# Kernel tuning notes

Hardware: AMD Instinct MI355X
Metric: run time of the kernel (lower is better)

The kernel has to match this reference:

```python
import jax, jax.numpy as jnp
import numpy as np

N_NODES = 100000
N_HYPEREDGES = 20000
NNZ = 600000
D = 128


def setup_inputs() -> dict:
    key = jax.random.key(0)
    k = jax.random.split(key, 6)
    s = 1.0 / np.sqrt(D)
    x = jax.random.normal(k[0], (N_NODES, D), jnp.float32)
    node_idx = jax.random.randint(k[1], (NNZ,), 0, N_NODES, dtype=jnp.int64 if jax.config.jax_enable_x64 else jnp.int32)
    edge_idx = jax.random.randint(k[2], (NNZ,), 0, N_HYPEREDGES, dtype=jnp.int64 if jax.config.jax_enable_x64 else jnp.int32)
    conv_W = jax.random.uniform(k[3], (D, D), jnp.float32, -s, s)
    conv_b = jnp.zeros((D,), jnp.float32)
    res_W = jax.random.uniform(k[4], (D, D), jnp.float32, -s, s)
    res_b = jax.random.uniform(k[5], (D,), jnp.float32, -s, s)
    return {"x": x, "node_idx": node_idx, "edge_idx": edge_idx,
            "conv_W": conv_W, "conv_b": conv_b, "res_W": res_W, "res_b": res_b}


def hypergraph_conv(x, node_idx, edge_idx, W, b):
    # PyG HypergraphConv (no attention, unit hyperedge weights):
    #   out = D^{-1} H B^{-1} H^T (x W) + b
    y = x @ W                                                      # [N, D]
    ones = jnp.ones(node_idx.shape, dtype=y.dtype)
    deg_n = jax.ops.segment_sum(ones, node_idx, num_segments=N_NODES)        # node degree
    deg_e = jax.ops.segment_sum(ones, edge_idx, num_segments=N_HYPEREDGES)   # hyperedge size
    inv_n = jnp.where(deg_n > 0, 1.0 / deg_n, 0.0)
    inv_e = jnp.where(deg_e > 0, 1.0 / deg_e, 0.0)
    # node -> hyperedge aggregation, normalized by B^{-1}
    e_feat = jax.ops.segment_sum(y[node_idx], edge_idx, num_segments=N_HYPEREDGES)
    e_feat = e_feat * inv_e[:, None]                               # [E, D]
    # hyperedge -> node aggregation, normalized by D^{-1}
    out = jax.ops.segment_sum(e_feat[edge_idx], node_idx, num_segments=N_NODES)
    out = out * inv_n[:, None]                                     # [N, D]
    return out + b


def reference(x, node_idx, edge_idx, conv_W, conv_b, res_W, res_b):
    h = hypergraph_conv(x, node_idx, edge_idx, conv_W, conv_b)     # layer_num = 1
    return (x @ res_W + res_b) + h                                 # residual Linear + conv out
```

## Files before the change

kernel.cpp:

```cpp
#include <hip/hip_runtime.h>

#define N_NODES 100000
#define N_EDGES 20000
#define NNZ_C   600000
#define D 128

typedef short bf16x8 __attribute__((ext_vector_type(8)));
typedef float f32x4  __attribute__((ext_vector_type(4)));

__device__ __forceinline__ unsigned short f2bf(float f) {
    unsigned int u = __float_as_uint(f);
    u = (u + 0x7fffu + ((u >> 16) & 1u)) >> 16;
    return (unsigned short)u;
}
__device__ __forceinline__ float bf2f(unsigned short h) {
    return __uint_as_float((unsigned int)h << 16);
}
__device__ __forceinline__ unsigned int pk_trunc(float lo, float hi) {
    return __builtin_amdgcn_perm(__float_as_uint(hi), __float_as_uint(lo),
                                 0x07060302);
}

#define CH 2048
#define NCHUNK 293
#define EBW 32
#define NBE 625
#define ECAP 1280
#define NBW 128
#define NBN 782
#define NCAP 1024
#define PADI 32
#define GCUR_INTS ((NBE + NBN) * PADI)

#define GT 64
#define XPAD 136
#define NTILES ((N_NODES + GT - 1) / GT)
#define GEMM_BLKS ((NTILES + 1) / 2)

__device__ __forceinline__ void stage_tile(unsigned short* __restrict__ buf,
                                           const float* __restrict__ x,
                                           int tile, int r0, int qp) {
    int n = tile * GT + r0;
    if (n >= N_NODES) n = N_NODES - 1;
    const float* xr = x + (size_t)n * D + qp * 16;
    unsigned short* dst = buf + r0 * XPAD + qp * 16;
#pragma unroll
    for (int u = 0; u < 2; ++u) {
        const float4 a = *(const float4*)(xr + u * 8);
        const float4 c = *(const float4*)(xr + u * 8 + 4);
        uint4 v;
        v.x = pk_trunc(a.x, a.y);
        v.y = pk_trunc(a.z, a.w);
        v.z = pk_trunc(c.x, c.y);
        v.w = pk_trunc(c.z, c.w);
        *(uint4*)(dst + u * 8) = v;
    }
}

__device__ __forceinline__ void compute_tile(
    const unsigned short* __restrict__ buf, const bf16x8 (&A)[2][4],
    int tile, int mat, int fh, int quad, int l16,
    unsigned short* __restrict__ yb, unsigned short* __restrict__ resb) {
    f32x4 acc[4][2] = {};
#pragma unroll
    for (int g = 0; g < 4; ++g)
#pragma unroll
        for (int kc = 0; kc < 4; ++kc) {
            const bf16x8 B = *(const bf16x8*)(buf + (g * 16 + l16) * XPAD +
                                              kc * 32 + quad * 8);
            acc[g][0] = __builtin_amdgcn_mfma_f32_16x16x32_bf16(A[0][kc], B, acc[g][0], 0, 0, 0);
            acc[g][1] = __builtin_amdgcn_mfma_f32_16x16x32_bf16(A[1][kc], B, acc[g][1], 0, 0, 0);
        }
    const int nbase = tile * GT;
    unsigned short* dst = mat ? resb : yb;
#pragma unroll
    for (int g = 0; g < 4; ++g) {
        const int n = nbase + g * 16 + l16;
        if (n >= N_NODES) continue;
#pragma unroll
        for (int ft = 0; ft < 2; ++ft) {
            const int f0 = fh + ft * 16 + quad * 4;
            uint2 v;
            v.x = pk_trunc(acc[g][ft][0], acc[g][ft][1]);
            v.y = pk_trunc(acc[g][ft][2], acc[g][ft][3]);
            *(uint2*)(dst + (size_t)n * D + f0) = v;
        }
    }
}

__global__ __launch_bounds__(512) void fused_bin_gemm(
    const float* __restrict__ x,
    const int* __restrict__ nidx, const int* __restrict__ eidx,
    const float* __restrict__ cW, const float* __restrict__ rW,
    unsigned short* __restrict__ yb, unsigned short* __restrict__ resb,
    int* __restrict__ bucket_e, int* __restrict__ bucket_n,
    int* __restrict__ gcur_e, int* __restrict__ gcur_n) {
    __shared__ int lds[10816];
    const int bid = blockIdx.x;
    const int tid = threadIdx.x;

    if (bid < NCHUNK) {
        int* rawE  = lds;
        int* rawN  = lds + 2048;
        int* srt   = lds + 4096;
        int* red   = lds + 6144;
        int* cnt   = lds + 6656;
        int* lbase = lds + 7438;
        int* gbase = lds + 8220;
        int* cur   = lds + 9002;
        unsigned short* sbin = (unsigned short*)(lds + 9784);
        const int j0 = bid * CH;
        const int jn = (j0 + CH < NNZ_C) ? CH : NNZ_C - j0;
        for (int i = tid; i < jn; i += 512) {
            rawE[i] = eidx[j0 + i];
            rawN[i] = nidx[j0 + i];
        }
        __syncthreads();
#pragma unroll
        for (int s = 0; s < 2; ++s) {
            const int nb = s ? NBN : NBE;
            int* gc = s ? gcur_n : gcur_e;
            int* dst = s ? bucket_n : bucket_e;
            const int cap = s ? NCAP : ECAP;
            for (int i = tid; i < nb; i += 512) cnt[i] = 0;
            __syncthreads();
            for (int i = tid; i < jn; i += 512)
                atomicAdd(&cnt[s ? (rawN[i] >> 7) : (rawE[i] >> 5)], 1);
            __syncthreads();
            const int i0 = tid * 2, i1 = tid * 2 + 1;
            const int a0 = (i0 < nb) ? cnt[i0] : 0;
            const int a1 = (i1 < nb) ? cnt[i1] : 0;
            const int sum = a0 + a1;
            red[tid] = sum;
            __syncthreads();
            for (int off = 1; off < 512; off <<= 1) {
                const int t = (tid >= off) ? red[tid - off] : 0;
                __syncthreads();
                red[tid] += t;
                __syncthreads();
            }
            const int excl = red[tid] - sum;
            if (i0 < nb) {
                lbase[i0] = excl; cur[i0] = excl;
                gbase[i0] = a0 ? atomicAdd(&gc[i0 * PADI], a0) : 0;
            }
            if (i1 < nb) {
                lbase[i1] = excl + a0; cur[i1] = excl + a0;
                gbase[i1] = a1 ? atomicAdd(&gc[i1 * PADI], a1) : 0;
            }
            __syncthreads();
            for (int i = tid; i < jn; i += 512) {
                const int e = rawE[i], n = rawN[i];
                const int b = s ? (n >> 7) : (e >> 5);
                const int pk = s ? (((n & 127) << 15) | e)
                                 : (((e & 31) << 17) | n);
                const int pos = atomicAdd(&cur[b], 1);
                srt[pos] = pk;
                sbin[pos] = (unsigned short)b;
            }
            __syncthreads();
            for (int i = tid; i < jn; i += 512) {
                const int b = sbin[i];
                const int o2 = gbase[b] + (i - lbase[b]);
                if (o2 < cap) dst[b * cap + o2] = srt[i];
            }
            __syncthreads();
        }
        return;
    }

    unsigned short* xs0 = (unsigned short*)lds;
    unsigned short* xs1 = xs0 + GT * XPAD;

    const int w    = tid >> 6;
    const int lane = tid & 63;
    const int quad = lane >> 4;
    const int l16  = lane & 15;
    const int mat  = w & 1;
    const int fh   = (w >> 1) * 32;
    const int r0 = tid >> 3;
    const int qp = tid & 7;
    const int t0 = (bid - NCHUNK) * 2;

    stage_tile(xs0, x, t0, r0, qp);

    const float* wf = mat ? rW : cW;
    bf16x8 A[2][4];
#pragma unroll
    for (int ft = 0; ft < 2; ++ft) {
        const int f = fh + ft * 16 + l16;
#pragma unroll
        for (int kc = 0; kc < 4; ++kc)
#pragma unroll
            for (int u = 0; u < 8; ++u)
                A[ft][kc][u] = (short)f2bf(wf[(kc * 32 + quad * 8 + u) * D + f]);
    }
    __syncthreads();
    stage_tile(xs1, x, t0 + 1, r0, qp);
    compute_tile(xs0, A, t0, mat, fh, quad, l16, yb, resb);
    __syncthreads();
    compute_tile(xs1, A, t0 + 1, mat, fh, quad, l16, yb, resb);
}

__global__ __launch_bounds__(512) void edge_aggregate(
    const int* __restrict__ bucket_e, const int* __restrict__ gcur_e,
    const unsigned short* __restrict__ yb, unsigned short* __restrict__ efb) {
    __shared__ int raw[ECAP];
    __shared__ int srt[ECAP];
    __shared__ int cnt[EBW + 1];
    __shared__ int cur[EBW];
    const int tid = threadIdx.x;
    const int b = blockIdx.x;
    int W = gcur_e[b * PADI];
    if (W > ECAP) W = ECAP;
    if (tid <= EBW) cnt[tid] = 0;
    __syncthreads();
    const int* src = bucket_e + b * ECAP;
    for (int i = tid; i < W; i += 512) {
        const int p = src[i];
        raw[i] = p;
        atomicAdd(&cnt[p >> 17], 1);
    }
    __syncthreads();
    if (tid < EBW) {
        const int c = cnt[tid];
        int v = c;
#pragma unroll
        for (int off = 1; off < EBW; off <<= 1) {
            const int t = __shfl_up(v, off);
            if (tid >= off) v += t;
        }
        cnt[tid] = v - c;
        cur[tid] = v - c;
        if (tid == EBW - 1) cnt[EBW] = v;
    }
    __syncthreads();
    for (int i = tid; i < W; i += 512) {
        const int p = raw[i];
        const int pos = atomicAdd(&cur[p >> 17], 1);
        srt[pos] = p & 0x1FFFF;
    }
    __syncthreads();

    const int g = tid >> 4;
    const int l = tid & 15;
    const int beg = cnt[g], end = cnt[g + 1];
    float acc[8] = {};
    int j = beg;
    for (; j + 4 <= end; j += 4) {
        const int n0 = srt[j], n1 = srt[j + 1];
        const int n2 = srt[j + 2], n3 = srt[j + 3];
        const bf16x8 p0 = *(const bf16x8*)(yb + (size_t)n0 * D + l * 8);
        const bf16x8 p1 = *(const bf16x8*)(yb + (size_t)n1 * D + l * 8);
        const bf16x8 p2 = *(const bf16x8*)(yb + (size_t)n2 * D + l * 8);
        const bf16x8 p3 = *(const bf16x8*)(yb + (size_t)n3 * D + l * 8);
#pragma unroll
        for (int i = 0; i < 8; ++i)
            acc[i] += (bf2f((unsigned short)p0[i]) + bf2f((unsigned short)p1[i]))
                    + (bf2f((unsigned short)p2[i]) + bf2f((unsigned short)p3[i]));
    }
    for (; j < end; ++j) {
        const bf16x8 p = *(const bf16x8*)(yb + (size_t)srt[j] * D + l * 8);
#pragma unroll
        for (int i = 0; i < 8; ++i) acc[i] += bf2f((unsigned short)p[i]);
    }
    const int deg = end - beg;
    const float inv = deg ? 1.f / (float)deg : 0.f;
    bf16x8 o;
#pragma unroll
    for (int i = 0; i < 8; ++i) o[i] = (short)f2bf(acc[i] * inv);
    *(bf16x8*)(efb + (size_t)(b * EBW + g) * D + l * 8) = o;
}

__global__ __launch_bounds__(512) void node_aggregate(
    const int* __restrict__ bucket_n, const int* __restrict__ gcur_n,
    const unsigned short* __restrict__ efb, const unsigned short* __restrict__ resb,
    const float* __restrict__ rb, const float* __restrict__ cb,
    float* __restrict__ out) {
    __shared__ int raw[NCAP];
    __shared__ int srt[NCAP];
    __shared__ int cnt[NBW + 1];
    __shared__ int cur[NBW];
    __shared__ int red[512];
    const int tid = threadIdx.x;
    const int b = blockIdx.x;
    int W = gcur_n[b * PADI];
    if (W > NCAP) W = NCAP;
    if (tid <= NBW) cnt[tid] = 0;
    __syncthreads();
    const int* src = bucket_n + b * NCAP;
    for (int i = tid; i < W; i += 512) {
        const int p = src[i];
        raw[i] = p;
        atomicAdd(&cnt[p >> 15], 1);
    }
    __syncthreads();
    const int v = (tid < NBW) ? cnt[tid] : 0;
    red[tid] = v;
    __syncthreads();
    for (int off = 1; off < 512; off <<= 1) {
        const int t = (tid >= off) ? red[tid - off] : 0;
        __syncthreads();
        red[tid] += t;
        __syncthreads();
    }
    const int excl = red[tid] - v;
    if (tid < NBW) { cnt[tid] = excl; cur[tid] = excl; }
    if (tid == NBW - 1) cnt[NBW] = red[tid];
    __syncthreads();
    for (int i = tid; i < W; i += 512) {
        const int p = raw[i];
        const int pos = atomicAdd(&cur[p >> 15], 1);
        srt[pos] = p & 0x7FFF;
    }
    __syncthreads();

    const int g = tid >> 4;
    const int l = tid & 15;
    const float4 rb0 = *(const float4*)(rb + l * 8);
    const float4 rb1 = *(const float4*)(rb + l * 8 + 4);
    const float4 cb0 = *(const float4*)(cb + l * 8);
    const float4 cb1 = *(const float4*)(cb + l * 8 + 4);
#pragma unroll
    for (int u = 0; u < 4; ++u) {
        const int nl = g * 4 + u;
        const int n = b * NBW + nl;
        if (n >= N_NODES) continue;
        const int beg = cnt[nl], end = cnt[nl + 1];
        float acc[8] = {};
        int j = beg;
        for (; j + 2 <= end; j += 2) {
            const int e0 = srt[j], e1 = srt[j + 1];
            const bf16x8 p0 = *(const bf16x8*)(efb + (size_t)e0 * D + l * 8);
            const bf16x8 p1 = *(const bf16x8*)(efb + (size_t)e1 * D + l * 8);
#pragma unroll
            for (int i = 0; i < 8; ++i)
                acc[i] += bf2f((unsigned short)p0[i]) + bf2f((unsigned short)p1[i]);
        }
        if (j < end) {
            const bf16x8 p = *(const bf16x8*)(efb + (size_t)srt[j] * D + l * 8);
#pragma unroll
            for (int i = 0; i < 8; ++i) acc[i] += bf2f((unsigned short)p[i]);
        }
        const int deg = end - beg;
        const float inv = deg ? 1.f / (float)deg : 0.f;
        const bf16x8 r = *(const bf16x8*)(resb + (size_t)n * D + l * 8);
        float4 o0, o1;
        o0.x = bf2f((unsigned short)r[0]) + acc[0] * inv + rb0.x + cb0.x;
        o0.y = bf2f((unsigned short)r[1]) + acc[1] * inv + rb0.y + cb0.y;
        o0.z = bf2f((unsigned short)r[2]) + acc[2] * inv + rb0.z + cb0.z;
        o0.w = bf2f((unsigned short)r[3]) + acc[3] * inv + rb0.w + cb0.w;
        o1.x = bf2f((unsigned short)r[4]) + acc[4] * inv + rb1.x + cb1.x;
        o1.y = bf2f((unsigned short)r[5]) + acc[5] * inv + rb1.y + cb1.y;
        o1.z = bf2f((unsigned short)r[6]) + acc[6] * inv + rb1.z + cb1.z;
        o1.w = bf2f((unsigned short)r[7]) + acc[7] * inv + rb1.w + cb1.w;
        const size_t o = (size_t)n * D + l * 8;
        *(float4*)(out + o) = o0;
        *(float4*)(out + o + 4) = o1;
    }
}

extern "C" void kernel_launch(void* const* d_in, const int* in_sizes, int n_in,
                              void* d_out, int out_size, void* d_ws,
                              size_t ws_size, hipStream_t stream) {
    const float* x  = (const float*)d_in[0];
    const int* nidx = (const int*)d_in[1];
    const int* eidx = (const int*)d_in[2];
    const float* cW = (const float*)d_in[3];
    const float* cb = (const float*)d_in[4];
    const float* rW = (const float*)d_in[5];
    const float* rb = (const float*)d_in[6];
    float* out = (float*)d_out;

    char* ws = (char*)d_ws;
    size_t off = 0;
    auto alloc = [&](size_t bytes) {
        size_t o = off;
        off += (bytes + 255) & ~(size_t)255;
        return o;
    };
    unsigned short* yb   = (unsigned short*)(ws + alloc((size_t)N_NODES * D * 2));
    unsigned short* resb = (unsigned short*)(ws + alloc((size_t)N_NODES * D * 2));
    unsigned short* efb  = (unsigned short*)(ws + alloc((size_t)N_EDGES * D * 2));
    int* bucket_e = (int*)(ws + alloc((size_t)NBE * ECAP * 4));
    int* bucket_n = (int*)(ws + alloc((size_t)NBN * NCAP * 4));
    int* gcur     = (int*)(ws + alloc((size_t)GCUR_INTS * 4));
    int* gcur_e = gcur;
    int* gcur_n = gcur + NBE * PADI;

    hipMemsetAsync(gcur, 0, (size_t)GCUR_INTS * 4, stream);

    fused_bin_gemm<<<NCHUNK + GEMM_BLKS, 512, 0, stream>>>(
        x, nidx, eidx, cW, rW, yb, resb,
        bucket_e, bucket_n, gcur_e, gcur_n);

    edge_aggregate<<<NBE, 512, 0, stream>>>(bucket_e, gcur_e, yb, efb);
    node_aggregate<<<NBN, 512, 0, stream>>>(bucket_n, gcur_n, efb, resb,
                                            rb, cb, out);
}
```

Measured before the change: 197.9 us.

## Aggregate raw bf16 features first and apply both GEMMs in one final pass

Uses linearity to move the conv weight multiply after both mean aggregations. The first kernel now only bins indices and converts x to bf16, the two gather kernels average raw features, and a final MFMA kernel computes z·Wc + x·Wr + biases in one pass. This removes the separate yb/resb buffers and the residual re-read in the node kernel, but adds a zb write and read plus an extra launch. The binning chunk size is also doubled, and the block scans now use warp shuffles instead of LDS-based scans.

```diff
diff --git a/kernel.cpp b/kernel.cpp
--- a/kernel.cpp
+++ b/kernel.cpp
@@ -21,8 +21,9 @@
                                  0x07060302);
 }
 
-#define CH 2048
-#define NCHUNK 293
+#define CH 4096
+#define NCHUNK 147
+#define CONVB 256
 #define EBW 32
 #define NBE 625
 #define ECAP 1280
@@ -35,176 +36,103 @@
 #define GT 64
 #define XPAD 136
 #define NTILES ((N_NODES + GT - 1) / GT)
-#define GEMM_BLKS ((NTILES + 1) / 2)
-
-__device__ __forceinline__ void stage_tile(unsigned short* __restrict__ buf,
-                                           const float* __restrict__ x,
-                                           int tile, int r0, int qp) {
-    int n = tile * GT + r0;
-    if (n >= N_NODES) n = N_NODES - 1;
-    const float* xr = x + (size_t)n * D + qp * 16;
-    unsigned short* dst = buf + r0 * XPAD + qp * 16;
-#pragma unroll
-    for (int u = 0; u < 2; ++u) {
-        const float4 a = *(const float4*)(xr + u * 8);
-        const float4 c = *(const float4*)(xr + u * 8 + 4);
-        uint4 v;
-        v.x = pk_trunc(a.x, a.y);
-        v.y = pk_trunc(a.z, a.w);
-        v.z = pk_trunc(c.x, c.y);
-        v.w = pk_trunc(c.z, c.w);
-        *(uint4*)(dst + u * 8) = v;
-    }
-}
-
-__device__ __forceinline__ void compute_tile(
-    const unsigned short* __restrict__ buf, const bf16x8 (&A)[2][4],
-    int tile, int mat, int fh, int quad, int l16,
-    unsigned short* __restrict__ yb, unsigned short* __restrict__ resb) {
-    f32x4 acc[4][2] = {};
-#pragma unroll
-    for (int g = 0; g < 4; ++g)
-#pragma unroll
-        for (int kc = 0; kc < 4; ++kc) {
-            const bf16x8 B = *(const bf16x8*)(buf + (g * 16 + l16) * XPAD +
-                                              kc * 32 + quad * 8);
-            acc[g][0] = __builtin_amdgcn_mfma_f32_16x16x32_bf16(A[0][kc], B, acc[g][0], 0, 0, 0);
-            acc[g][1] = __builtin_amdgcn_mfma_f32_16x16x32_bf16(A[1][kc], B, acc[g][1], 0, 0, 0);
-        }
-    const int nbase = tile * GT;
-    unsigned short* dst = mat ? resb : yb;
-#pragma unroll
-    for (int g = 0; g < 4; ++g) {
-        const int n = nbase + g * 16 + l16;
-        if (n >= N_NODES) continue;
-#pragma unroll
-        for (int ft = 0; ft < 2; ++ft) {
-            const int f0 = fh + ft * 16 + quad * 4;
-            uint2 v;
-            v.x = pk_trunc(acc[g][ft][0], acc[g][ft][1]);
-            v.y = pk_trunc(acc[g][ft][2], acc[g][ft][3]);
-            *(uint2*)(dst + (size_t)n * D + f0) = v;
-        }
-    }
-}
-
-__global__ __launch_bounds__(512) void fused_bin_gemm(
+#define TPB 3
+#define GEMM_BLKS ((NTILES + TPB - 1) / TPB)
+
+__global__ __launch_bounds__(512) void fused_bin_conv(
     const float* __restrict__ x,
     const int* __restrict__ nidx, const int* __restrict__ eidx,
-    const float* __restrict__ cW, const float* __restrict__ rW,
-    unsigned short* __restrict__ yb, unsigned short* __restrict__ resb,
+    unsigned short* __restrict__ xb,
     int* __restrict__ bucket_e, int* __restrict__ bucket_n,
     int* __restrict__ gcur_e, int* __restrict__ gcur_n) {
-    __shared__ int lds[10816];
+    __shared__ int srt[CH];
+    __shared__ int cnt[NBN], lbase[NBN], gbase[NBN], cur[NBN];
     const int bid = blockIdx.x;
     const int tid = threadIdx.x;
 
-    if (bid < NCHUNK) {
-        int* rawE  = lds;
-        int* rawN  = lds + 2048;
-        int* srt   = lds + 4096;
-        int* red   = lds + 6144;
-        int* cnt   = lds + 6656;
-        int* lbase = lds + 7438;
-        int* gbase = lds + 8220;
-        int* cur   = lds + 9002;
-        unsigned short* sbin = (unsigned short*)(lds + 9784);
-        const int j0 = bid * CH;
-        const int jn = (j0 + CH < NNZ_C) ? CH : NNZ_C - j0;
+    if (bid >= NCHUNK) {
+        const int total8 = N_NODES * D / 8;
+        for (int g = (bid - NCHUNK) * 512 + tid; g < total8;
+             g += CONVB * 512) {
+            const float4 a = *(const float4*)(x + (size_t)g * 8);
+            const float4 c = *(const float4*)(x + (size_t)g * 8 + 4);
+            uint4 v;
+            v.x = pk_trunc(a.x, a.y);
+            v.y = pk_trunc(a.z, a.w);
+            v.z = pk_trunc(c.x, c.y);
+            v.w = pk_trunc(c.z, c.w);
+            *(uint4*)(xb + (size_t)g * 8) = v;
+        }
+        return;
+    }
+
+    const int j0 = bid * CH;
+    const int jn = (j0 + CH < NNZ_C) ? CH : NNZ_C - j0;
+#pragma unroll
+    for (int s = 0; s < 2; ++s) {
+        const int nb = s ? NBN : NBE;
+        int* gc = s ? gcur_n : gcur_e;
+        int* dst = s ? bucket_n : bucket_e;
+        const int cap = s ? NCAP : ECAP;
+        for (int i = tid; i < nb; i += 512) cnt[i] = 0;
+        __syncthreads();
         for (int i = tid; i < jn; i += 512) {
-            rawE[i] = eidx[j0 + i];
-            rawN[i] = nidx[j0 + i];
-        }
-        __syncthreads();
-#pragma unroll
-        for (int s = 0; s < 2; ++s) {
-            const int nb = s ? NBN : NBE;
-            int* gc = s ? gcur_n : gcur_e;
-            int* dst = s ? bucket_n : bucket_e;
-            const int cap = s ? NCAP : ECAP;
-            for (int i = tid; i < nb; i += 512) cnt[i] = 0;
-            __syncthreads();
-            for (int i = tid; i < jn; i += 512)
-                atomicAdd(&cnt[s ? (rawN[i] >> 7) : (rawE[i] >> 5)], 1);
-            __syncthreads();
-            const int i0 = tid * 2, i1 = tid * 2 + 1;
-            const int a0 = (i0 < nb) ? cnt[i0] : 0;
-            const int a1 = (i1 < nb) ? cnt[i1] : 0;
-            const int sum = a0 + a1;
-            red[tid] = sum;
-            __syncthreads();
-            for (int off = 1; off < 512; off <<= 1) {
-                const int t = (tid >= off) ? red[tid - off] : 0;
-                __syncthreads();
-                red[tid] += t;
-                __syncthreads();
+            const int id = s ? nidx[j0 + i] : eidx[j0 + i];
+            atomicAdd(&cnt[s ? (id >> 7) : (id >> 5)], 1);
+        }
+        __syncthreads();
+        if (tid < 64) {
+            int loc[13];
+            int ssum = 0;
+            const int k0 = tid * 13;
+#pragma unroll
+            for (int k = 0; k < 13; ++k) {
+                const int idx = k0 + k;
+                loc[k] = ssum;
+                if (idx < nb) ssum += cnt[idx];
             }
-            const int excl = red[tid] - sum;
-            if (i0 < nb) {
-                lbase[i0] = excl; cur[i0] = excl;
-                gbase[i0] = a0 ? atomicAdd(&gc[i0 * PADI], a0) : 0;
+            int v = ssum;
+#pragma unroll
+            for (int off = 1; off < 64; off <<= 1) {
+                const int t = __shfl_up(v, off);
+                if (tid >= off) v += t;
             }
-            if (i1 < nb) {
-                lbase[i1] = excl + a0; cur[i1] = excl + a0;
-                gbase[i1] = a1 ? atomicAdd(&gc[i1 * PADI], a1) : 0;
+            const int base = v - ssum;
+#pragma unroll
+            for (int k = 0; k < 13; ++k) {
+                const int idx = k0 + k;
+                if (idx < nb) {
+                    lbase[idx] = base + loc[k];
+                    cur[idx] = base + loc[k];
+                }
             }
-            __syncthreads();
-            for (int i = tid; i < jn; i += 512) {
-                const int e = rawE[i], n = rawN[i];
-                const int b = s ? (n >> 7) : (e >> 5);
-                const int pk = s ? (((n & 127) << 15) | e)
-                                 : (((e & 31) << 17) | n);
-                const int pos = atomicAdd(&cur[b], 1);
-                srt[pos] = pk;
-                sbin[pos] = (unsigned short)b;
-            }
-            __syncthreads();
-            for (int i = tid; i < jn; i += 512) {
-                const int b = sbin[i];
-                const int o2 = gbase[b] + (i - lbase[b]);
-                if (o2 < cap) dst[b * cap + o2] = srt[i];
-            }
-            __syncthreads();
-        }
-        return;
-    }
-
-    unsigned short* xs0 = (unsigned short*)lds;
-    unsigned short* xs1 = xs0 + GT * XPAD;
-
-    const int w    = tid >> 6;
-    const int lane = tid & 63;
-    const int quad = lane >> 4;
-    const int l16  = lane & 15;
-    const int mat  = w & 1;
-    const int fh   = (w >> 1) * 32;
-    const int r0 = tid >> 3;
-    const int qp = tid & 7;
-    const int t0 = (bid - NCHUNK) * 2;
-
-    stage_tile(xs0, x, t0, r0, qp);
-
-    const float* wf = mat ? rW : cW;
-    bf16x8 A[2][4];
-#pragma unroll
-    for (int ft = 0; ft < 2; ++ft) {
-        const int f = fh + ft * 16 + l16;
-#pragma unroll
-        for (int kc = 0; kc < 4; ++kc)
-#pragma unroll
-            for (int u = 0; u < 8; ++u)
-                A[ft][kc][u] = (short)f2bf(wf[(kc * 32 + quad * 8 + u) * D + f]);
-    }
-    __syncthreads();
-    stage_tile(xs1, x, t0 + 1, r0, qp);
-    compute_tile(xs0, A, t0, mat, fh, quad, l16, yb, resb);
-    __syncthreads();
-    compute_tile(xs1, A, t0 + 1, mat, fh, quad, l16, yb, resb);
-}
-
-__global__ __launch_bounds__(512) void edge_aggregate(
+        }
+        __syncthreads();
+        for (int i = tid; i < nb; i += 512)
+            gbase[i] = cnt[i] ? atomicAdd(&gc[i * PADI], cnt[i]) : 0;
+        __syncthreads();
+        for (int i = tid; i < jn; i += 512) {
+            const int e = eidx[j0 + i], n = nidx[j0 + i];
+            const int b = s ? (n >> 7) : (e >> 5);
+            const unsigned pk = s ? (unsigned)(((n & 127) << 15) | e)
+                                  : (unsigned)(((e & 31) << 17) | n);
+            const int pos = atomicAdd(&cur[b], 1);
+            srt[pos] = (int)(pk | ((unsigned)b << 22));
+        }
+        __syncthreads();
+        for (int i = tid; i < jn; i += 512) {
+            const unsigned v = (unsigned)srt[i];
+            const int b = v >> 22;
+            const int o2 = gbase[b] + (i - lbase[b]);
+            if (o2 < cap) dst[b * cap + o2] = (int)(v & 0x3FFFFFu);
+        }
+        __syncthreads();
+    }
+}
+
+__global__ __launch_bounds__(512) void edge_mean(
     const int* __restrict__ bucket_e, const int* __restrict__ gcur_e,
-    const unsigned short* __restrict__ yb, unsigned short* __restrict__ efb) {
+    const unsigned short* __restrict__ xb, unsigned short* __restrict__ sb) {
     __shared__ int raw[ECAP];
     __shared__ int srt[ECAP];
     __shared__ int cnt[EBW + 1];
@@ -250,17 +178,17 @@
     for (; j + 4 <= end; j += 4) {
         const int n0 = srt[j], n1 = srt[j + 1];
         const int n2 = srt[j + 2], n3 = srt[j + 3];
-        const bf16x8 p0 = *(const bf16x8*)(yb + (size_t)n0 * D + l * 8);
-        const bf16x8 p1 = *(const bf16x8*)(yb + (size_t)n1 * D + l * 8);
-        const bf16x8 p2 = *(const bf16x8*)(yb + (size_t)n2 * D + l * 8);
-        const bf16x8 p3 = *(const bf16x8*)(yb + (size_t)n3 * D + l * 8);
+        const bf16x8 p0 = *(const bf16x8*)(xb + (size_t)n0 * D + l * 8);
+        const bf16x8 p1 = *(const bf16x8*)(xb + (size_t)n1 * D + l * 8);
+        const bf16x8 p2 = *(const bf16x8*)(xb + (size_t)n2 * D + l * 8);
+        const bf16x8 p3 = *(const bf16x8*)(xb + (size_t)n3 * D + l * 8);
 #pragma unroll
         for (int i = 0; i < 8; ++i)
             acc[i] += (bf2f((unsigned short)p0[i]) + bf2f((unsigned short)p1[i]))
                     + (bf2f((unsigned short)p2[i]) + bf2f((unsigned short)p3[i]));
     }
     for (; j < end; ++j) {
-        const bf16x8 p = *(const bf16x8*)(yb + (size_t)srt[j] * D + l * 8);
+        const bf16x8 p = *(const bf16x8*)(xb + (size_t)srt[j] * D + l * 8);
 #pragma unroll
         for (int i = 0; i < 8; ++i) acc[i] += bf2f((unsigned short)p[i]);
     }
@@ -269,19 +197,16 @@
     bf16x8 o;
 #pragma unroll
     for (int i = 0; i < 8; ++i) o[i] = (short)f2bf(acc[i] * inv);
-    *(bf16x8*)(efb + (size_t)(b * EBW + g) * D + l * 8) = o;
-}
-
-__global__ __launch_bounds__(512) void node_aggregate(
+    *(bf16x8*)(sb + (size_t)(b * EBW + g) * D + l * 8) = o;
+}
+
+__global__ __launch_bounds__(512) void node_mean(
     const int* __restrict__ bucket_n, const int* __restrict__ gcur_n,
-    const unsigned short* __restrict__ efb, const unsigned short* __restrict__ resb,
-    const float* __restrict__ rb, const float* __restrict__ cb,
-    float* __restrict__ out) {
+    const unsigned short* __restrict__ sb, unsigned short* __restrict__ zb) {
     __shared__ int raw[NCAP];
     __shared__ int srt[NCAP];
     __shared__ int cnt[NBW + 1];
     __shared__ int cur[NBW];
-    __shared__ int red[512];
     const int tid = threadIdx.x;
     const int b = blockIdx.x;
     int W = gcur_n[b * PADI];
@@ -295,18 +220,20 @@
         atomicAdd(&cnt[p >> 15], 1);
     }
     __syncthreads();
-    const int v = (tid < NBW) ? cnt[tid] : 0;
-    red[tid] = v;
-    __syncthreads();
-    for (int off = 1; off < 512; off <<= 1) {
-        const int t = (tid >= off) ? red[tid - off] : 0;
-        __syncthreads();
-        red[tid] += t;
-        __syncthreads();
-    }
-    const int excl = red[tid] - v;
-    if (tid < NBW) { cnt[tid] = excl; cur[tid] = excl; }
-    if (tid == NBW - 1) cnt[NBW] = red[tid];
+    if (tid < 64) {
+        const int a0 = cnt[tid * 2], a1 = cnt[tid * 2 + 1];
+        const int ssum = a0 + a1;
+        int v = ssum;
+#pragma unroll
+        for (int off = 1; off < 64; off <<= 1) {
+            const int t = __shfl_up(v, off);
+            if (tid >= off) v += t;
+        }
+        const int base = v - ssum;
+        cnt[tid * 2] = base;     cur[tid * 2] = base;
+        cnt[tid * 2 + 1] = base + a0; cur[tid * 2 + 1] = base + a0;
+        if (tid == 63) cnt[NBW] = v;
+    }
     __syncthreads();
     for (int i = tid; i < W; i += 512) {
         const int p = raw[i];
@@ -317,10 +244,6 @@
 
     const int g = tid >> 4;
     const int l = tid & 15;
-    const float4 rb0 = *(const float4*)(rb + l * 8);
-    const float4 rb1 = *(const float4*)(rb + l * 8 + 4);
-    const float4 cb0 = *(const float4*)(cb + l * 8);
-    const float4 cb1 = *(const float4*)(cb + l * 8 + 4);
 #pragma unroll
     for (int u = 0; u < 4; ++u) {
         const int nl = g * 4 + u;
@@ -331,32 +254,97 @@
         int j = beg;
         for (; j + 2 <= end; j += 2) {
             const int e0 = srt[j], e1 = srt[j + 1];
-            const bf16x8 p0 = *(const bf16x8*)(efb + (size_t)e0 * D + l * 8);
-            const bf16x8 p1 = *(const bf16x8*)(efb + (size_t)e1 * D + l * 8);
+            const bf16x8 p0 = *(const bf16x8*)(sb + (size_t)e0 * D + l * 8);
+            const bf16x8 p1 = *(const bf16x8*)(sb + (size_t)e1 * D + l * 8);
 #pragma unroll
             for (int i = 0; i < 8; ++i)
                 acc[i] += bf2f((unsigned short)p0[i]) + bf2f((unsigned short)p1[i]);
         }
         if (j < end) {
-            const bf16x8 p = *(const bf16x8*)(efb + (size_t)srt[j] * D + l * 8);
+            const bf16x8 p = *(const bf16x8*)(sb + (size_t)srt[j] * D + l * 8);
 #pragma unroll
             for (int i = 0; i < 8; ++i) acc[i] += bf2f((unsigned short)p[i]);
         }
         const int deg = end - beg;
         const float inv = deg ? 1.f / (float)deg : 0.f;
-        const bf16x8 r = *(const bf16x8*)(resb + (size_t)n * D + l * 8);
-        float4 o0, o1;
-        o0.x = bf2f((unsigned short)r[0]) + acc[0] * inv + rb0.x + cb0.x;
-        o0.y = bf2f((unsigned short)r[1]) + acc[1] * inv + rb0.y + cb0.y;
-        o0.z = bf2f((unsigned short)r[2]) + acc[2] * inv + rb0.z + cb0.z;
-        o0.w = bf2f((unsigned short)r[3]) + acc[3] * inv + rb0.w + cb0.w;
-        o1.x = bf2f((unsigned short)r[4]) + acc[4] * inv + rb1.x + cb1.x;
-        o1.y = bf2f((unsigned short)r[5]) + acc[5] * inv + rb1.y + cb1.y;
-        o1.z = bf2f((unsigned short)r[6]) + acc[6] * inv + rb1.z + cb1.z;
-        o1.w = bf2f((unsigned short)r[7]) + acc[7] * inv + rb1.w + cb1.w;
-        const size_t o = (size_t)n * D + l * 8;
-        *(float4*)(out + o) = o0;
-        *(float4*)(out + o + 4) = o1;
+        bf16x8 o;
+#pragma unroll
+        for (int i = 0; i < 8; ++i) o[i] = (short)f2bf(acc[i] * inv);
+        *(bf16x8*)(zb + (size_t)n * D + l * 8) = o;
+    }
+}
+
+__global__ __launch_bounds__(512) void final_gemm(
+    const unsigned short* __restrict__ zb, const unsigned short* __restrict__ xb,
+    const float* __restrict__ cW, const float* __restrict__ rW,
+    const float* __restrict__ cbias, const float* __restrict__ rbias,
+    float* __restrict__ out) {
+    __shared__ unsigned short zs[GT * XPAD];
+    __shared__ unsigned short xs[GT * XPAD];
+
+    const int tid  = threadIdx.x;
+    const int w    = tid >> 6;
+    const int lane = tid & 63;
+    const int quad = lane >> 4;
+    const int l16  = lane & 15;
+    const int f0   = w * 16;
+
+    const int f = f0 + l16;
+    bf16x8 Ac[4], Ar[4];
+#pragma unroll
+    for (int kc = 0; kc < 4; ++kc)
+#pragma unroll
+        for (int u = 0; u < 8; ++u) {
+            const int k = kc * 32 + quad * 8 + u;
+            Ac[kc][u] = (short)f2bf(cW[(size_t)k * D + f]);
+            Ar[kc][u] = (short)f2bf(rW[(size_t)k * D + f]);
+        }
+    const float4 cb4 = *(const float4*)(cbias + f0 + quad * 4);
+    const float4 rb4 = *(const float4*)(rbias + f0 + quad * 4);
+    const float4 bias = {cb4.x + rb4.x, cb4.y + rb4.y,
+                         cb4.z + rb4.z, cb4.w + rb4.w};
+
+    const int r0 = tid >> 3;
+    const int qp = tid & 7;
+
+    for (int tt = 0; tt < TPB; ++tt) {
+        const int t = blockIdx.x * TPB + tt;
+        if (t >= NTILES) break;
+        __syncthreads();
+        {
+            int n = t * GT + r0;
+            if (n >= N_NODES) n = N_NODES - 1;
+            const uint4* sz = (const uint4*)(zb + (size_t)n * D + qp * 16);
+            const uint4* sx = (const uint4*)(xb + (size_t)n * D + qp * 16);
+            uint4* dz = (uint4*)(zs + r0 * XPAD + qp * 16);
+            uint4* dx = (uint4*)(xs + r0 * XPAD + qp * 16);
+            dz[0] = sz[0]; dz[1] = sz[1];
+            dx[0] = sx[0]; dx[1] = sx[1];
+        }
+        __syncthreads();
+        f32x4 acc[4] = {};
+#pragma unroll
+        for (int g = 0; g < 4; ++g)
+#pragma unroll
+            for (int kc = 0; kc < 4; ++kc) {
+                const int ro = (g * 16 + l16) * XPAD + kc * 32 + quad * 8;
+                const bf16x8 Bz = *(const bf16x8*)(zs + ro);
+                const bf16x8 Bx = *(const bf16x8*)(xs + ro);
+                acc[g] = __builtin_amdgcn_mfma_f32_16x16x32_bf16(Ac[kc], Bz, acc[g], 0, 0, 0);
+                acc[g] = __builtin_amdgcn_mfma_f32_16x16x32_bf16(Ar[kc], Bx, acc[g], 0, 0, 0);
+            }
+        const int nbase = t * GT;
+#pragma unroll
+        for (int g = 0; g < 4; ++g) {
+            const int n = nbase + g * 16 + l16;
+            if (n >= N_NODES) continue;
+            float4 o;
+            o.x = acc[g][0] + bias.x;
+            o.y = acc[g][1] + bias.y;
+            o.z = acc[g][2] + bias.z;
+            o.w = acc[g][3] + bias.w;
+            *(float4*)(out + (size_t)n * D + f0 + quad * 4) = o;
+        }
     }
 }
 
@@ -379,9 +367,9 @@
         off += (bytes + 255) & ~(size_t)255;
         return o;
     };
-    unsigned short* yb   = (unsigned short*)(ws + alloc((size_t)N_NODES * D * 2));
-    unsigned short* resb = (unsigned short*)(ws + alloc((size_t)N_NODES * D * 2));
-    unsigned short* efb  = (unsigned short*)(ws + alloc((size_t)N_EDGES * D * 2));
+    unsigned short* xb = (unsigned short*)(ws + alloc((size_t)N_NODES * D * 2));
+    unsigned short* sb = (unsigned short*)(ws + alloc((size_t)N_EDGES * D * 2));
+    unsigned short* zb = (unsigned short*)(ws + alloc((size_t)N_NODES * D * 2));
     int* bucket_e = (int*)(ws + alloc((size_t)NBE * ECAP * 4));
     int* bucket_n = (int*)(ws + alloc((size_t)NBN * NCAP * 4));
     int* gcur     = (int*)(ws + alloc((size_t)GCUR_INTS * 4));
@@ -390,11 +378,10 @@
 
     hipMemsetAsync(gcur, 0, (size_t)GCUR_INTS * 4, stream);
 
-    fused_bin_gemm<<<NCHUNK + GEMM_BLKS, 512, 0, stream>>>(
-        x, nidx, eidx, cW, rW, yb, resb,
-        bucket_e, bucket_n, gcur_e, gcur_n);
-
-    edge_aggregate<<<NBE, 512, 0, stream>>>(bucket_e, gcur_e, yb, efb);
-    node_aggregate<<<NBN, 512, 0, stream>>>(bucket_n, gcur_n, efb, resb,
-                                            rb, cb, out);
-}
+    fused_bin_conv<<<NCHUNK + CONVB, 512, 0, stream>>>(
+        x, nidx, eidx, xb, bucket_e, bucket_n, gcur_e, gcur_n);
+
+    edge_mean<<<NBE, 512, 0, stream>>>(bucket_e, gcur_e, xb, sb);
+    node_mean<<<NBN, 512, 0, stream>>>(bucket_n, gcur_n, sb, zb);
+    final_gemm<<<GEMM_BLKS, 512, 0, stream>>>(zb, xb, cW, rW, cb, rb, out);
+}
```

After: 193.3 us. -2.4%, faster.
